# Kernel tuning notes

Hardware: AMD Instinct MI355X
Metric: run time of the kernel (lower is better)

The kernel has to match this reference:

```python
import jax, jax.numpy as jnp
import numpy as np

N_NODES = 50000
N_EDGES = 600000
D_IN = 128
HIDDEN = 128
N_REL = 8
N_LAYERS = 2


def setup_inputs() -> dict:
    key = jax.random.key(0)
    ks = jax.random.split(key, 10)
    node_feat = jax.random.normal(ks[0], (N_NODES, D_IN), dtype=jnp.float32)
    edge_index = jax.random.randint(ks[1], (2, N_EDGES), 0, N_NODES, dtype=jnp.int64)
    edge_type = jax.random.randint(ks[2], (N_EDGES,), 0, N_REL, dtype=jnp.int64)
    s = 1.0 / np.sqrt(D_IN)
    # stacked per-layer FastRGCNConv params (input_dim == hidden so shapes match)
    rel_w = jax.random.normal(ks[3], (N_LAYERS, N_REL, D_IN, HIDDEN), dtype=jnp.float32) * s
    root_w = jax.random.normal(ks[4], (N_LAYERS, D_IN, HIDDEN), dtype=jnp.float32) * s
    bias = jax.random.normal(ks[5], (N_LAYERS, HIDDEN), dtype=jnp.float32) * 0.01
    proj_w = jax.random.normal(ks[6], (N_LAYERS * HIDDEN, HIDDEN), dtype=jnp.float32) / np.sqrt(N_LAYERS * HIDDEN)
    proj_b = jax.random.normal(ks[7], (HIDDEN,), dtype=jnp.float32) * 0.01
    return {
        "node_feat": node_feat,
        "edge_index": edge_index,
        "edge_type": edge_type,
        "rel_w": rel_w,
        "root_w": root_w,
        "bias": bias,
        "proj_w": proj_w,
        "proj_b": proj_b,
    }


def _rgcn_layer(x, src, dst, etype, W, root, b):
    # FastRGCNConv: transform all nodes by all relations, then gather per edge.
    xW = jnp.einsum('nd,rdh->nrh', x, W)          # [N, R, H]
    m = xW[src, etype]                             # [E, H] per-edge message
    # mean aggregation per (target, relation), as in PyG FastRGCNConv aggr='mean'
    seg = dst * N_REL + etype                      # combined (target, relation) id
    cnt = jax.ops.segment_sum(jnp.ones_like(etype, dtype=x.dtype), seg,
                              num_segments=N_NODES * N_REL)
    norm = (1.0 / jnp.clip(cnt, 1.0, None))[seg]   # [E]
    agg = jax.ops.segment_sum(m * norm[:, None], dst, num_segments=N_NODES)
    return agg + x @ root + b


def reference(node_feat, edge_index, edge_type, rel_w, root_w, bias, proj_w, proj_b):
    src, dst = edge_index[0], edge_index[1]
    reps = []
    h = node_feat
    for i in range(N_LAYERS):
        h = _rgcn_layer(h, src, dst, edge_type, rel_w[i], root_w[i], bias[i])
        h = jax.nn.relu(h)
        reps.append(h)
    final = jnp.concatenate(reps, axis=-1) @ proj_w + proj_b
    return (final,) + tuple(reps)
```

## Files before the change

kernel.cpp:

```cpp
#include <hip/hip_runtime.h>
#include <hip/hip_bf16.h>

#define NN 50000
#define NE 600000
#define DD 128
#define RR 8
#define KA 1152

#define N2 (NN * RR)
#define SCHUNK 1024
#define NBS2 ((N2 + SCHUNK - 1) / SCHUNK)

typedef __attribute__((ext_vector_type(8))) short short8;
typedef __attribute__((ext_vector_type(4))) float f32x4;

__device__ __forceinline__ unsigned short f2b(float x){
  __hip_bfloat16 h = __float2bfloat16(x);
  return __builtin_bit_cast(unsigned short, h);
}
__device__ __forceinline__ float blo(unsigned u){ return __builtin_bit_cast(float, u << 16); }
__device__ __forceinline__ float bhi(unsigned u){ return __builtin_bit_cast(float, u & 0xFFFF0000u); }
__device__ __forceinline__ unsigned pack2(float a, float b){
  return (unsigned)f2b(a) | ((unsigned)f2b(b) << 16);
}

#define GLDS16(g, l) __builtin_amdgcn_global_load_lds( \
    (const __attribute__((address_space(1))) void*)(g), \
    (__attribute__((address_space(3))) void*)(l), 16, 0, 0)

__global__ __launch_bounds__(256) void k_hist(const int* __restrict__ ei,
                                              const int* __restrict__ et,
                                              int* __restrict__ cnt_vr) {
  int e = blockIdx.x * 256 + threadIdx.x;
  if (e < NE) {
    int dst = ei[NE + e];
    int r = et[e];
    atomicAdd(&cnt_vr[dst * RR + r], 1);
  }
}

__global__ __launch_bounds__(256) void k_scan1(const int* __restrict__ cnt,
                                               int* __restrict__ bsum) {
  int b = blockIdx.x, t = threadIdx.x;
  int base = b * SCHUNK + t * 4;
  int s = 0;
  if (base < N2) {
    int4 v = *(const int4*)&cnt[base];
    s = v.x + v.y + v.z + v.w;
  }
  #pragma unroll
  for (int off = 32; off; off >>= 1) s += __shfl_down(s, off);
  __shared__ int wsum[4];
  int lane = t & 63, wv = t >> 6;
  if (lane == 0) wsum[wv] = s;
  __syncthreads();
  if (t == 0) bsum[b] = wsum[0] + wsum[1] + wsum[2] + wsum[3];
}

__global__ __launch_bounds__(512) void k_scan2(const int* __restrict__ bsum,
                                               int* __restrict__ boff) {
  int t = threadIdx.x, lane = t & 63, wv = t >> 6;
  int v = (t < NBS2) ? bsum[t] : 0;
  int x = v;
  #pragma unroll
  for (int off = 1; off < 64; off <<= 1) {
    int y = __shfl_up(x, off);
    if (lane >= off) x += y;
  }
  __shared__ int wt[8];
  if (lane == 63) wt[wv] = x;
  __syncthreads();
  int woff = 0;
  for (int w = 0; w < wv; w++) woff += wt[w];
  if (t < NBS2) boff[t] = woff + x - v;
}

__global__ __launch_bounds__(256) void k_scan3(const int* __restrict__ cnt,
                                               const int* __restrict__ boff,
                                               int* __restrict__ rp2,
                                               int* __restrict__ cur2) {
  int b = blockIdx.x, t = threadIdx.x;
  int lane = t & 63, wv = t >> 6;
  int base = b * SCHUNK + t * 4;
  int v[4] = {0, 0, 0, 0};
  int s = 0;
  if (base < N2) {
    int4 q = *(const int4*)&cnt[base];
    v[0] = q.x; v[1] = q.y; v[2] = q.z; v[3] = q.w;
    s = q.x + q.y + q.z + q.w;
  }
  int x = s;
  #pragma unroll
  for (int off = 1; off < 64; off <<= 1) {
    int y = __shfl_up(x, off);
    if (lane >= off) x += y;
  }
  __shared__ int wtot[4];
  if (lane == 63) wtot[wv] = x;
  __syncthreads();
  int woff = 0;
  for (int w = 0; w < wv; w++) woff += wtot[w];
  int exc = boff[b] + woff + x - s;
  if (base < N2) {
    #pragma unroll
    for (int j = 0; j < 4; j++) {
      cur2[base + j] = exc;
      rp2[base + j + 1] = exc + v[j];
      exc += v[j];
    }
  }
  if (b == 0 && t == 0) rp2[0] = 0;
}

__global__ __launch_bounds__(256) void k_scatter(const int* __restrict__ ei,
                                                 const int* __restrict__ et,
                                                 int* __restrict__ cur2,
                                                 unsigned short* __restrict__ psrc) {
  int e = blockIdx.x * 256 + threadIdx.x;
  if (e < NE) {
    int src = ei[e];
    int dst = ei[NE + e];
    int r = et[e];
    int p = atomicAdd(&cur2[dst * RR + r], 1);
    psrc[p] = (unsigned short)src;
  }
}

__global__ __launch_bounds__(256) void k_xb(const float* __restrict__ x,
                                            unsigned* __restrict__ xb2) {
  int i = blockIdx.x * 256 + threadIdx.x;
  if (i < NN * (DD / 2)) {
    float2 v = ((const float2*)x)[i];
    xb2[i] = pack2(v.x, v.y);
  }
}

__global__ __launch_bounds__(256) void k_wt(const float* __restrict__ rel_w,
                                            const float* __restrict__ root_w,
                                            unsigned short* __restrict__ WT) {
  int idx = blockIdx.x * 256 + threadIdx.x;
  if (idx >= 2 * DD * KA) return;
  int k = idx % KA;
  int n = (idx / KA) % DD;
  int l = idx / (KA * DD);
  float v;
  if (k < RR * DD) v = rel_w[((size_t)l * RR * DD + k) * DD + n];
  else             v = root_w[((size_t)l * DD + (k - RR * DD)) * DD + n];
  WT[idx] = f2b(v);
}

__global__ __launch_bounds__(256) void k_pt(const float* __restrict__ proj_w,
                                            unsigned short* __restrict__ PT) {
  int idx = blockIdx.x * 256 + threadIdx.x;
  if (idx >= DD * 256) return;
  int k = idx % 256;
  int n = idx / 256;
  PT[idx] = f2b(proj_w[(size_t)k * DD + n]);
}

__global__ __launch_bounds__(256) void k_agg(const unsigned short* __restrict__ xb, int xstride,
                                             const unsigned short* __restrict__ psrc,
                                             const int* __restrict__ rp2,
                                             unsigned short* __restrict__ A2) {
  int v = blockIdx.x * 4 + (threadIdx.x >> 6);
  int l = threadIdx.x & 63;
  if (v >= NN) return;
  int b = 0;
  if (l < 9) b = rp2[v * RR + l];
  unsigned* row = (unsigned*)(A2 + (size_t)v * KA);
  unsigned xs = *(const unsigned*)(xb + (size_t)v * xstride + 2 * l);
  #pragma unroll
  for (int rr = 0; rr < RR; rr++) {
    int e0 = __shfl(b, rr), e1 = __shfl(b, rr + 1);
    float a0 = 0.f, a1 = 0.f;
    for (int e = e0; e < e1; e++) {
      int src = psrc[e];
      unsigned u = *(const unsigned*)(xb + (size_t)src * xstride + 2 * l);
      a0 += blo(u); a1 += bhi(u);
    }
    float s = (e1 > e0) ? 1.f / (float)(e1 - e0) : 0.f;
    row[rr * 64 + l] = pack2(a0 * s, a1 * s);
  }
  row[RR * 64 + l] = xs;
}

__global__ __launch_bounds__(256) void k_gemm(const unsigned short* __restrict__ A, int lda,
                                              const unsigned short* __restrict__ BT, int ldb,
                                              int M, int K,
                                              const float* __restrict__ bias,
                                              float* __restrict__ outf,
                                              unsigned short* __restrict__ hb, int hboff,
                                              int dorelu) {
  __shared__ unsigned short sA[128 * 64];
  __shared__ unsigned short sB[128 * 64];
  int t = threadIdx.x;
  int bm = blockIdx.x;
  int lane = t & 63, wv = t >> 6;
  int wm = wv >> 1, wn = wv & 1;
  int l15 = lane & 15, lk = lane >> 4;

  f32x4 acc[4][4];
  #pragma unroll
  for (int mi = 0; mi < 4; mi++)
    #pragma unroll
    for (int ni = 0; ni < 4; ni++)
      acc[mi][ni] = (f32x4){0.f, 0.f, 0.f, 0.f};

  int nkt = K >> 6;
  for (int kt = 0; kt < nkt; kt++) {
    #pragma unroll
    for (int i = 0; i < 4; i++) {
      int f = i * 256 + t;
      int row = f >> 3, cl = f & 7;
      int cg = cl ^ (row & 7);
      int rg = bm * 128 + row;
      if (rg >= M) rg = M - 1;
      const unsigned short* src = A + (size_t)rg * lda + kt * 64 + cg * 8;
      GLDS16(src, &sA[f * 8]);
    }
    #pragma unroll
    for (int i = 0; i < 4; i++) {
      int f = i * 256 + t;
      int row = f >> 3, cl = f & 7;
      int cg = cl ^ (row & 7);
      const unsigned short* src = BT + (size_t)row * ldb + kt * 64 + cg * 8;
      GLDS16(src, &sB[f * 8]);
    }
    __syncthreads();

    short8 af[4][2], bf[4][2];
    #pragma unroll
    for (int mi = 0; mi < 4; mi++) {
      #pragma unroll
      for (int kk = 0; kk < 2; kk++) {
        int r = wm * 64 + mi * 16 + l15;
        int c = kk * 4 + lk;
        af[mi][kk] = *(const short8*)&sA[((r << 3) + (c ^ (r & 7))) << 3];
        int rb = wn * 64 + mi * 16 + l15;
        bf[mi][kk] = *(const short8*)&sB[((rb << 3) + (c ^ (rb & 7))) << 3];
      }
    }
    #pragma unroll
    for (int mi = 0; mi < 4; mi++)
      #pragma unroll
      for (int ni = 0; ni < 4; ni++)
        #pragma unroll
        for (int kk = 0; kk < 2; kk++)
          acc[mi][ni] = __builtin_amdgcn_mfma_f32_16x16x32_bf16(af[mi][kk], bf[ni][kk], acc[mi][ni], 0, 0, 0);
    __syncthreads();
  }

  #pragma unroll
  for (int mi = 0; mi < 4; mi++) {
    #pragma unroll
    for (int ni = 0; ni < 4; ni++) {
      int cg = wn * 64 + ni * 16 + l15;
      float bv = bias[cg];
      #pragma unroll
      for (int j = 0; j < 4; j++) {
        int rg = bm * 128 + wm * 64 + mi * 16 + lk * 4 + j;
        if (rg < M) {
          float val = acc[mi][ni][j] + bv;
          if (dorelu) val = fmaxf(val, 0.f);
          outf[(size_t)rg * 128 + cg] = val;
          if (hb) hb[(size_t)rg * 256 + hboff + cg] = f2b(val);
        }
      }
    }
  }
}

extern "C" void kernel_launch(void* const* d_in, const int* in_sizes, int n_in,
                              void* d_out, int out_size, void* d_ws, size_t ws_size,
                              hipStream_t stream) {
  const float* node_feat = (const float*)d_in[0];
  const int*   ei        = (const int*)d_in[1];
  const int*   et        = (const int*)d_in[2];
  const float* rel_w     = (const float*)d_in[3];
  const float* root_w    = (const float*)d_in[4];
  const float* bias      = (const float*)d_in[5];
  const float* proj_w    = (const float*)d_in[6];
  const float* proj_b    = (const float*)d_in[7];
  float* out = (float*)d_out;

  char* ws = (char*)d_ws;
  size_t off = 0;
  auto carve = [&](size_t bytes) { void* p = ws + off; off = (off + bytes + 255) & ~(size_t)255; return p; };
  unsigned short* A2   = (unsigned short*)carve((size_t)NN * KA * 2);
  unsigned short* Hb   = (unsigned short*)carve((size_t)NN * 256 * 2);
  unsigned short* xb   = (unsigned short*)carve((size_t)NN * DD * 2);
  unsigned short* WT   = (unsigned short*)carve((size_t)2 * DD * KA * 2);
  unsigned short* PT   = (unsigned short*)carve((size_t)DD * 256 * 2);
  int* cnt_vr          = (int*)carve((size_t)N2 * 4);
  int* rp2             = (int*)carve((size_t)(N2 + 1) * 4);
  int* cur2            = (int*)carve((size_t)N2 * 4);
  unsigned short* psrc = (unsigned short*)carve((size_t)NE * 2);
  int* bsum            = (int*)carve((size_t)512 * 4);
  int* boff            = (int*)carve((size_t)512 * 4);
  (void)ws_size; (void)in_sizes; (void)n_in; (void)out_size;

  hipMemsetAsync(cnt_vr, 0, (size_t)N2 * 4, stream);

  int egrid = (NE + 255) / 256;
  k_hist<<<egrid, 256, 0, stream>>>(ei, et, cnt_vr);
  k_scan1<<<NBS2, 256, 0, stream>>>(cnt_vr, bsum);
  k_scan2<<<1, 512, 0, stream>>>(bsum, boff);
  k_scan3<<<NBS2, 256, 0, stream>>>(cnt_vr, boff, rp2, cur2);
  k_scatter<<<egrid, 256, 0, stream>>>(ei, et, cur2, psrc);

  k_xb<<<(NN * (DD / 2) + 255) / 256, 256, 0, stream>>>(node_feat, (unsigned*)xb);
  k_wt<<<(2 * DD * KA + 255) / 256, 256, 0, stream>>>(rel_w, root_w, WT);
  k_pt<<<(DD * 256 + 255) / 256, 256, 0, stream>>>(proj_w, PT);

  int mgrid = (NN + 127) / 128;

  k_agg<<<(NN + 3) / 4, 256, 0, stream>>>(xb, DD, psrc, rp2, A2);
  k_gemm<<<mgrid, 256, 0, stream>>>(A2, KA, WT, KA, NN, KA, bias,
                                    out + (size_t)NN * DD, Hb, 0, 1);

  k_agg<<<(NN + 3) / 4, 256, 0, stream>>>(Hb, 256, psrc, rp2, A2);
  k_gemm<<<mgrid, 256, 0, stream>>>(A2, KA, WT + (size_t)DD * KA, KA, NN, KA, bias + DD,
                                    out + (size_t)2 * NN * DD, Hb, DD, 1);

  k_gemm<<<mgrid, 256, 0, stream>>>(Hb, 256, PT, 256, NN, 256, proj_b,
                                    out, (unsigned short*)nullptr, 0, 0);
}
```

Before: 308.9 us.

## Fuse neighbor aggregation into per-layer GEMM and switch to relation-major CSR

Replaces the separate aggregation kernel and the layer GEMM with one kernel. For each relation, the kernel gathers and mean-aggregates neighbor features for a 128-node tile directly into shared memory, then runs the MFMA tile product against that relation's weight slice. This removes the large intermediate A2 buffer and its write and read traffic in global memory. The CSR counters are reorganised relation-major so each wave can read contiguous edge ranges for its 32 nodes, and caches source indices in LDS when they fit. In exchange, the irregular gathers now run inside a low-occupancy GEMM-sized grid (about 391 blocks with large shared-memory use), so gather latency may be poorly hidden.

After: 880.7 us. 2.85x slower.

```diff
diff --git a/kernel.cpp b/kernel.cpp
--- a/kernel.cpp
+++ b/kernel.cpp
@@ -30,12 +30,12 @@
 
 __global__ __launch_bounds__(256) void k_hist(const int* __restrict__ ei,
                                               const int* __restrict__ et,
-                                              int* __restrict__ cnt_vr) {
+                                              int* __restrict__ cnt) {
   int e = blockIdx.x * 256 + threadIdx.x;
   if (e < NE) {
     int dst = ei[NE + e];
     int r = et[e];
-    atomicAdd(&cnt_vr[dst * RR + r], 1);
+    atomicAdd(&cnt[r * NN + dst], 1);
   }
 }
 
@@ -121,7 +121,7 @@
     int src = ei[e];
     int dst = ei[NE + e];
     int r = et[e];
-    int p = atomicAdd(&cur2[dst * RR + r], 1);
+    int p = atomicAdd(&cur2[r * NN + dst], 1);
     psrc[p] = (unsigned short)src;
   }
 }
@@ -158,39 +158,132 @@
   PT[idx] = f2b(proj_w[(size_t)k * DD + n]);
 }
 
-__global__ __launch_bounds__(256) void k_agg(const unsigned short* __restrict__ xb, int xstride,
-                                             const unsigned short* __restrict__ psrc,
-                                             const int* __restrict__ rp2,
-                                             unsigned short* __restrict__ A2) {
-  int v = blockIdx.x * 4 + (threadIdx.x >> 6);
-  int l = threadIdx.x & 63;
-  if (v >= NN) return;
-  int b = 0;
-  if (l < 9) b = rp2[v * RR + l];
-  unsigned* row = (unsigned*)(A2 + (size_t)v * KA);
-  unsigned xs = *(const unsigned*)(xb + (size_t)v * xstride + 2 * l);
-  #pragma unroll
-  for (int rr = 0; rr < RR; rr++) {
-    int e0 = __shfl(b, rr), e1 = __shfl(b, rr + 1);
-    float a0 = 0.f, a1 = 0.f;
-    for (int e = e0; e < e1; e++) {
-      int src = psrc[e];
-      unsigned u = *(const unsigned*)(xb + (size_t)src * xstride + 2 * l);
-      a0 += blo(u); a1 += bhi(u);
-    }
-    float s = (e1 > e0) ? 1.f / (float)(e1 - e0) : 0.f;
-    row[rr * 64 + l] = pack2(a0 * s, a1 * s);
-  }
-  row[RR * 64 + l] = xs;
+__global__ __launch_bounds__(256) void k_layer(
+    const unsigned short* __restrict__ xb, int xstride,
+    const unsigned short* __restrict__ psrc,
+    const int* __restrict__ rp2,
+    const unsigned short* __restrict__ BT,
+    const float* __restrict__ bias,
+    float* __restrict__ outf,
+    unsigned short* __restrict__ hb, int hboff)
+{
+  __shared__ unsigned short smA[128 * 128];
+  __shared__ unsigned short smB[128 * 128];
+  __shared__ unsigned short sE[4][1024];
+  int t = threadIdx.x, bm = blockIdx.x;
+  int lane = t & 63, wv = t >> 6;
+  int wm = wv >> 1, wn = wv & 1;
+  int l15 = lane & 15, lk = lane >> 4;
+  int vbase = bm * 128 + wv * 32;
+
+  f32x4 acc[4][4];
+  #pragma unroll
+  for (int mi = 0; mi < 4; mi++)
+    #pragma unroll
+    for (int ni = 0; ni < 4; ni++)
+      acc[mi][ni] = (f32x4){0.f, 0.f, 0.f, 0.f};
+
+  for (int rr = 0; rr < 9; rr++) {
+    #pragma unroll
+    for (int i = 0; i < 8; i++) {
+      int f = i * 256 + t;
+      int row = f >> 4, cl = f & 15;
+      int cg = cl ^ (row & 15);
+      GLDS16(BT + (size_t)row * KA + rr * 128 + cg * 8, &smB[f * 8]);
+    }
+
+    if (rr < 8) {
+      int b = 0;
+      if (lane <= 32) {
+        int v = vbase + lane; if (v > NN) v = NN;
+        b = rp2[rr * NN + v];
+      }
+      int e_begin = __shfl(b, 0);
+      int e_end   = __shfl(b, 32);
+      int range = e_end - e_begin;
+      bool inlds = (range <= 1024);
+      if (inlds) {
+        for (int j = lane; j < range; j += 64) sE[wv][j] = psrc[e_begin + j];
+      }
+      for (int ii = 0; ii < 32; ii += 2) {
+        int e0A = __shfl(b, ii), e1A = __shfl(b, ii + 1), e1B = __shfl(b, ii + 2);
+        int eA = e0A, eB = e1A;
+        float aA0 = 0.f, aA1 = 0.f, aB0 = 0.f, aB1 = 0.f;
+        while (eA < e1A || eB < e1B) {
+          bool dA = eA < e1A, dB = eB < e1B;
+          unsigned uA = 0, uB = 0;
+          if (dA) {
+            int s = inlds ? sE[wv][eA - e_begin] : psrc[eA];
+            uA = *(const unsigned*)(xb + (size_t)s * xstride + 2 * lane);
+          }
+          if (dB) {
+            int s = inlds ? sE[wv][eB - e_begin] : psrc[eB];
+            uB = *(const unsigned*)(xb + (size_t)s * xstride + 2 * lane);
+          }
+          if (dA) { aA0 += blo(uA); aA1 += bhi(uA); eA++; }
+          if (dB) { aB0 += blo(uB); aB1 += bhi(uB); eB++; }
+        }
+        int cA = e1A - e0A, cB = e1B - e1A;
+        float fA = (cA > 0) ? 1.f / (float)cA : 0.f;
+        float fB = (cB > 0) ? 1.f / (float)cB : 0.f;
+        int rowA = wv * 32 + ii, rowB = rowA + 1;
+        ((unsigned*)smA)[rowA * 64 + ((((lane >> 2) ^ (rowA & 15)) << 2) | (lane & 3))] = pack2(aA0 * fA, aA1 * fA);
+        ((unsigned*)smA)[rowB * 64 + ((((lane >> 2) ^ (rowB & 15)) << 2) | (lane & 3))] = pack2(aB0 * fB, aB1 * fB);
+      }
+    } else {
+      for (int i = 0; i < 32; i++) {
+        int vg = vbase + i; if (vg >= NN) vg = NN - 1;
+        unsigned u = *(const unsigned*)(xb + (size_t)vg * xstride + 2 * lane);
+        int row = wv * 32 + i;
+        ((unsigned*)smA)[row * 64 + ((((lane >> 2) ^ (row & 15)) << 2) | (lane & 3))] = u;
+      }
+    }
+    __syncthreads();
+
+    #pragma unroll
+    for (int kk = 0; kk < 4; kk++) {
+      short8 af[4], bf[4];
+      #pragma unroll
+      for (int q = 0; q < 4; q++) {
+        int r  = wm * 64 + q * 16 + l15;
+        int rb = wn * 64 + q * 16 + l15;
+        int c  = kk * 4 + lk;
+        af[q] = *(const short8*)&smA[r * 128 + (((c ^ (r & 15))) << 3)];
+        bf[q] = *(const short8*)&smB[rb * 128 + (((c ^ (rb & 15))) << 3)];
+      }
+      #pragma unroll
+      for (int mi = 0; mi < 4; mi++)
+        #pragma unroll
+        for (int ni = 0; ni < 4; ni++)
+          acc[mi][ni] = __builtin_amdgcn_mfma_f32_16x16x32_bf16(af[mi], bf[ni], acc[mi][ni], 0, 0, 0);
+    }
+    __syncthreads();
+  }
+
+  #pragma unroll
+  for (int mi = 0; mi < 4; mi++) {
+    #pragma unroll
+    for (int ni = 0; ni < 4; ni++) {
+      int cg = wn * 64 + ni * 16 + l15;
+      float bv = bias[cg];
+      #pragma unroll
+      for (int j = 0; j < 4; j++) {
+        int rg = bm * 128 + wm * 64 + mi * 16 + lk * 4 + j;
+        if (rg < NN) {
+          float val = fmaxf(acc[mi][ni][j] + bv, 0.f);
+          outf[(size_t)rg * 128 + cg] = val;
+          hb[(size_t)rg * 256 + hboff + cg] = f2b(val);
+        }
+      }
+    }
+  }
 }
 
 __global__ __launch_bounds__(256) void k_gemm(const unsigned short* __restrict__ A, int lda,
                                               const unsigned short* __restrict__ BT, int ldb,
                                               int M, int K,
                                               const float* __restrict__ bias,
-                                              float* __restrict__ outf,
-                                              unsigned short* __restrict__ hb, int hboff,
-                                              int dorelu) {
+                                              float* __restrict__ outf) {
   __shared__ unsigned short sA[128 * 64];
   __shared__ unsigned short sB[128 * 64];
   int t = threadIdx.x;
@@ -215,16 +308,14 @@
       int cg = cl ^ (row & 7);
       int rg = bm * 128 + row;
       if (rg >= M) rg = M - 1;
-      const unsigned short* src = A + (size_t)rg * lda + kt * 64 + cg * 8;
-      GLDS16(src, &sA[f * 8]);
+      GLDS16(A + (size_t)rg * lda + kt * 64 + cg * 8, &sA[f * 8]);
     }
     #pragma unroll
     for (int i = 0; i < 4; i++) {
       int f = i * 256 + t;
       int row = f >> 3, cl = f & 7;
       int cg = cl ^ (row & 7);
-      const unsigned short* src = BT + (size_t)row * ldb + kt * 64 + cg * 8;
-      GLDS16(src, &sB[f * 8]);
+      GLDS16(BT + (size_t)row * ldb + kt * 64 + cg * 8, &sB[f * 8]);
     }
     __syncthreads();
 
@@ -259,12 +350,7 @@
       #pragma unroll
       for (int j = 0; j < 4; j++) {
         int rg = bm * 128 + wm * 64 + mi * 16 + lk * 4 + j;
-        if (rg < M) {
-          float val = acc[mi][ni][j] + bv;
-          if (dorelu) val = fmaxf(val, 0.f);
-          outf[(size_t)rg * 128 + cg] = val;
-          if (hb) hb[(size_t)rg * 256 + hboff + cg] = f2b(val);
-        }
+        if (rg < M) outf[(size_t)rg * 128 + cg] = acc[mi][ni][j] + bv;
       }
     }
   }
@@ -286,7 +372,6 @@
   char* ws = (char*)d_ws;
   size_t off = 0;
   auto carve = [&](size_t bytes) { void* p = ws + off; off = (off + bytes + 255) & ~(size_t)255; return p; };
-  unsigned short* A2   = (unsigned short*)carve((size_t)NN * KA * 2);
   unsigned short* Hb   = (unsigned short*)carve((size_t)NN * 256 * 2);
   unsigned short* xb   = (unsigned short*)carve((size_t)NN * DD * 2);
   unsigned short* WT   = (unsigned short*)carve((size_t)2 * DD * KA * 2);
@@ -314,14 +399,9 @@
 
   int mgrid = (NN + 127) / 128;
 
-  k_agg<<<(NN + 3) / 4, 256, 0, stream>>>(xb, DD, psrc, rp2, A2);
-  k_gemm<<<mgrid, 256, 0, stream>>>(A2, KA, WT, KA, NN, KA, bias,
-                                    out + (size_t)NN * DD, Hb, 0, 1);
-
-  k_agg<<<(NN + 3) / 4, 256, 0, stream>>>(Hb, 256, psrc, rp2, A2);
-  k_gemm<<<mgrid, 256, 0, stream>>>(A2, KA, WT + (size_t)DD * KA, KA, NN, KA, bias + DD,
-                                    out + (size_t)2 * NN * DD, Hb, DD, 1);
-
-  k_gemm<<<mgrid, 256, 0, stream>>>(Hb, 256, PT, 256, NN, 256, proj_b,
-                                    out, (unsigned short*)nullptr, 0, 0);
-}
+  k_layer<<<mgrid, 256, 0, stream>>>(xb, DD, psrc, rp2, WT, bias,
+                                     out + (size_t)NN * DD, Hb, 0);
+  k_layer<<<mgrid, 256, 0, stream>>>(Hb, 256, psrc, rp2, WT + (size_t)DD * KA, bias + DD,
+                                     out + (size_t)2 * NN * DD, Hb, DD);
+  k_gemm<<<mgrid, 256, 0, stream>>>(Hb, 256, PT, 256, NN, 256, proj_b, out);
+}
```
